# Performance work log

Measured on AMD Instinct MI355X. Metric: run time of the kernel, lower is better.

## Reference

```python
import jax, jax.numpy as jnp
import numpy as np

WIN = (2, 7, 7)  # (H, W, D) window size

def _relative_position_index(H, W, D):
    coords = np.stack(np.meshgrid(np.arange(H), np.arange(W), np.arange(D), indexing='ij'))
    cf = coords.reshape(3, -1)  # [3, N]
    rel = cf[:, :, None] - cf[:, None, :]  # [3, N, N]
    rel = rel.transpose(1, 2, 0).copy()
    rel[:, :, 0] += H - 1
    rel[:, :, 1] += W - 1
    rel[:, :, 2] += D - 1
    rel[:, :, 0] *= (2 * W - 1) * (2 * D - 1)
    rel[:, :, 1] *= 2 * D - 1
    return jnp.asarray(rel.sum(-1), dtype=jnp.int32)  # [N, N]

def setup_inputs() -> dict:
    key = jax.random.key(0)
    ks = jax.random.split(key, 7)
    H, W, D = WIN
    N = H * W * D          # 98
    C = 192
    nh = 6
    num_windows = 64
    B_ = 8 * num_windows   # 512
    x = jax.random.normal(ks[0], (B_, N, C), dtype=jnp.float32)
    # shifted-window attention mask: 0 for allowed pairs, -100 for masked
    mask = jnp.where(jax.random.uniform(ks[1], (num_windows, N, N)) < 0.9, 0.0, -100.0).astype(jnp.float32)
    qkv_w = jax.random.normal(ks[2], (3 * C, C), dtype=jnp.float32) * 0.02
    qkv_b = jnp.zeros((3 * C,), dtype=jnp.float32)
    out_w = jax.random.normal(ks[3], (C, C), dtype=jnp.float32) * 0.02
    out_b = jnp.zeros((C,), dtype=jnp.float32)
    table_len = (2 * H - 1) * (2 * W - 1) * (2 * D - 1)  # 507
    bias_table = jax.random.normal(ks[4], (table_len, nh), dtype=jnp.float32) * 0.02
    rel_index = _relative_position_index(H, W, D)
    return {"x": x, "mask": mask, "qkv_w": qkv_w, "qkv_b": qkv_b,
            "out_w": out_w, "out_b": out_b, "bias_table": bias_table,
            "rel_index": rel_index}

def reference(x, mask, qkv_w, qkv_b, out_w, out_b, bias_table, rel_index):
    B_, N, C = x.shape
    nh = bias_table.shape[1]
    d = C // nh
    scale = d ** (-0.5)
    qkv = (x @ qkv_w.T + qkv_b).reshape(B_, N, 3, nh, d)
    qkv = qkv.transpose(2, 0, 3, 1, 4)          # [3, B_, nh, N, d]
    q, k, v = qkv[0], qkv[1], qkv[2]
    attn = jnp.einsum('bhnd,bhmd->bhnm', q, k) * scale   # [B_, nh, N, N]
    bias = bias_table[rel_index]                 # [N, N, nh]
    attn = attn + bias.transpose(2, 0, 1)[None]  # add relative position bias
    nw = mask.shape[0]
    attn = attn.reshape(B_ // nw, nw, nh, N, N) + mask[None, :, None]
    attn = attn.reshape(B_, nh, N, N)
    p = jax.nn.softmax(attn, axis=-1)
    out = jnp.einsum('bhnm,bhmd->bhnd', p, v)    # [B_, nh, N, d]
    out = out.transpose(0, 2, 1, 3).reshape(B_, N, C)
    return out @ out_w.T + out_b
```

## Files before the change

### kernel.cpp

```cpp
#include <hip/hip_runtime.h>

typedef __attribute__((ext_vector_type(8))) __bf16 bf16x8;
typedef __attribute__((ext_vector_type(4))) float f32x4;
typedef __attribute__((ext_vector_type(8))) unsigned short us8;
typedef __attribute__((ext_vector_type(4))) unsigned short us4;

#define NTOK 98
#define NPAD 112
#define CDIM 192
#define NH 6
#define HD 32
#define NWIN 64
#define BWIN 512
#define MROWS (BWIN * NTOK)
#define QKVN (3 * CDIM)
#define SCALE 0.17677669529663687f

__device__ __forceinline__ unsigned short f2b(float f) {
  unsigned u = __builtin_bit_cast(unsigned, f);
  u += 0x7FFFu + ((u >> 16) & 1u);
  return (unsigned short)(u >> 16);
}

__device__ __forceinline__ bf16x8 ldfrag(const unsigned short* p) {
  return __builtin_bit_cast(bf16x8, *(const us8*)p);
}

__global__ __launch_bounds__(256) void k_biasmask(
    const float* __restrict__ mask, const float* __restrict__ table,
    const int* __restrict__ relidx, float* __restrict__ bm) {
  int idx = blockIdx.x * 256 + threadIdx.x;
  if (idx >= NWIN * NH * NTOK * NTOK) return;
  int j = idx % NTOK;
  int t = idx / NTOK;
  int i = t % NTOK;
  t /= NTOK;
  int h = t % NH;
  int w = t / NH;
  bm[idx] = table[relidx[i * NTOK + j] * NH + h] + mask[(w * NTOK + i) * NTOK + j];
}

__global__ __launch_bounds__(256) void k_qkv(
    const float* __restrict__ x, const float* __restrict__ w,
    const float* __restrict__ bias, unsigned short* __restrict__ qkv) {
  __shared__ unsigned short As[128 * 200];
  __shared__ unsigned short Bs[64 * 200];
  const int tid = threadIdx.x;
  const int m0 = blockIdx.x * 128;
  for (int it = 0; it < 24; ++it) {
    int q = it * 256 + tid;
    int row = q / 48, c4 = q - row * 48;
    float4 v = *(const float4*)(x + (m0 + row) * CDIM + c4 * 4);
    us4 u = {f2b(v.x), f2b(v.y), f2b(v.z), f2b(v.w)};
    *(us4*)&As[row * 200 + c4 * 4] = u;
  }
  const int lane = tid & 63;
  const int l15 = lane & 15, hi = lane >> 4;
  const int wr = (tid >> 6) >> 1, wc = (tid >> 6) & 1;
  __syncthreads();
  for (int j = 0; j < 9; ++j) {
    for (int it = 0; it < 12; ++it) {
      int q = it * 256 + tid;
      int row = q / 48, c4 = q - row * 48;
      float4 v = *(const float4*)(w + (j * 64 + row) * CDIM + c4 * 4);
      us4 u = {f2b(v.x), f2b(v.y), f2b(v.z), f2b(v.w)};
      *(us4*)&Bs[row * 200 + c4 * 4] = u;
    }
    __syncthreads();
    f32x4 acc[4][2];
#pragma unroll
    for (int fr = 0; fr < 4; ++fr) { acc[fr][0] = (f32x4)0.f; acc[fr][1] = (f32x4)0.f; }
#pragma unroll
    for (int ks = 0; ks < 6; ++ks) {
      int k0 = ks * 32 + hi * 8;
      bf16x8 b0 = ldfrag(&Bs[(wc * 32 + l15) * 200 + k0]);
      bf16x8 b1 = ldfrag(&Bs[(wc * 32 + 16 + l15) * 200 + k0]);
#pragma unroll
      for (int fr = 0; fr < 4; ++fr) {
        bf16x8 a = ldfrag(&As[(wr * 64 + fr * 16 + l15) * 200 + k0]);
        acc[fr][0] = __builtin_amdgcn_mfma_f32_16x16x32_bf16(a, b0, acc[fr][0], 0, 0, 0);
        acc[fr][1] = __builtin_amdgcn_mfma_f32_16x16x32_bf16(a, b1, acc[fr][1], 0, 0, 0);
      }
    }
    __syncthreads();
#pragma unroll
    for (int fr = 0; fr < 4; ++fr)
#pragma unroll
      for (int fc = 0; fc < 2; ++fc)
#pragma unroll
        for (int r = 0; r < 4; ++r) {
          int row = m0 + wr * 64 + fr * 16 + hi * 4 + r;
          int col = j * 64 + wc * 32 + fc * 16 + l15;
          float v = acc[fr][fc][r] + bias[col];
          if (col < CDIM) v *= SCALE;
          qkv[row * QKVN + col] = f2b(v);
        }
  }
}

__global__ __launch_bounds__(448) void k_attn(
    const unsigned short* __restrict__ qkv, const float* __restrict__ bm,
    unsigned short* __restrict__ ao) {
  __shared__ unsigned short Ks[NPAD * 40];
  __shared__ unsigned short Vt[32 * 136];
  __shared__ unsigned short P[NPAD * 136];
  const int tid = threadIdx.x;
  const int h = blockIdx.x % NH;
  const int b = blockIdx.x / NH;
  const int wnd = b & (NWIN - 1);
  const int lane = tid & 63, wv = tid >> 6;
  const int l15 = lane & 15, hi = lane >> 4;
  {
    int row = tid >> 2, q = tid & 3;
    us8 kv = (us8)0;
    if (row < NTOK)
      kv = *(const us8*)(qkv + (b * NTOK + row) * QKVN + CDIM + h * HD + q * 8);
    *(us8*)&Ks[row * 40 + q * 8] = kv;
    if (row < NTOK) {
      us8 vv = *(const us8*)(qkv + (b * NTOK + row) * QKVN + 2 * CDIM + h * HD + q * 8);
#pragma unroll
      for (int i = 0; i < 8; ++i) Vt[(q * 8 + i) * 136 + row] = vv[i];
    }
    for (int i = tid; i < 32 * 38; i += 448) {
      int dd = i / 38, n = NTOK + (i - dd * 38);
      Vt[dd * 136 + n] = 0;
    }
    for (int i = tid; i < NPAD * 16; i += 448)
      P[(i >> 4) * 136 + 112 + (i & 15)] = 0;
  }
  int qn = wv * 16 + l15;
  us8 qu = (us8)0;
  if (qn < NTOK)
    qu = *(const us8*)(qkv + (b * NTOK + qn) * QKVN + h * HD + hi * 8);
  bf16x8 qf = __builtin_bit_cast(bf16x8, qu);
  __syncthreads();
  f32x4 sacc[7];
#pragma unroll
  for (int tc = 0; tc < 7; ++tc) {
    bf16x8 kb = ldfrag(&Ks[(tc * 16 + l15) * 40 + hi * 8]);
    sacc[tc] = __builtin_amdgcn_mfma_f32_16x16x32_bf16(qf, kb, (f32x4)0.f, 0, 0, 0);
  }
  const float* bmp = bm + (wnd * NH + h) * NTOK * NTOK;
  float rsum[4];
#pragma unroll
  for (int r = 0; r < 4; ++r) {
    int row = wv * 16 + hi * 4 + r;
    float sv[7];
    float m = -1e30f;
#pragma unroll
    for (int tc = 0; tc < 7; ++tc) {
      int col = tc * 16 + l15;
      float val = -1e30f;
      if (col < NTOK && row < NTOK) val = sacc[tc][r] + bmp[row * NTOK + col];
      sv[tc] = val;
      m = fmaxf(m, val);
    }
#pragma unroll
    for (int off = 1; off < 16; off <<= 1) m = fmaxf(m, __shfl_xor(m, off));
    float s = 0.f;
#pragma unroll
    for (int tc = 0; tc < 7; ++tc) {
      float e = __expf(sv[tc] - m);
      s += e;
      P[row * 136 + tc * 16 + l15] = f2b(e);
    }
#pragma unroll
    for (int off = 1; off < 16; off <<= 1) s += __shfl_xor(s, off);
    rsum[r] = s;
  }
  f32x4 oacc[2];
  oacc[0] = (f32x4)0.f; oacc[1] = (f32x4)0.f;
#pragma unroll
  for (int ks = 0; ks < 4; ++ks) {
    int k0 = ks * 32 + hi * 8;
    bf16x8 pa = ldfrag(&P[(wv * 16 + l15) * 136 + k0]);
#pragma unroll
    for (int tc = 0; tc < 2; ++tc) {
      bf16x8 vb = ldfrag(&Vt[(tc * 16 + l15) * 136 + k0]);
      oacc[tc] = __builtin_amdgcn_mfma_f32_16x16x32_bf16(pa, vb, oacc[tc], 0, 0, 0);
    }
  }
#pragma unroll
  for (int tc = 0; tc < 2; ++tc)
#pragma unroll
    for (int r = 0; r < 4; ++r) {
      int row = wv * 16 + hi * 4 + r;
      if (row < NTOK) {
        float v = oacc[tc][r] / rsum[r];
        ao[(b * NTOK + row) * CDIM + h * HD + tc * 16 + l15] = f2b(v);
      }
    }
}

__global__ __launch_bounds__(256) void k_proj(
    const unsigned short* __restrict__ a, const float* __restrict__ w,
    const float* __restrict__ bias, float* __restrict__ out) {
  __shared__ unsigned short As[128 * 200];
  __shared__ unsigned short Bs[64 * 200];
  const int tid = threadIdx.x;
  const int m0 = blockIdx.x * 128;
  for (int it = 0; it < 12; ++it) {
    int q = it * 256 + tid;
    int row = q / 24, c8 = q - row * 24;
    *(us8*)&As[row * 200 + c8 * 8] = *(const us8*)(a + (m0 + row) * CDIM + c8 * 8);
  }
  const int lane = tid & 63;
  const int l15 = lane & 15, hi = lane >> 4;
  const int wr = (tid >> 6) >> 1, wc = (tid >> 6) & 1;
  __syncthreads();
  for (int j = 0; j < 3; ++j) {
    for (int it = 0; it < 12; ++it) {
      int q = it * 256 + tid;
      int row = q / 48, c4 = q - row * 48;
      float4 v = *(const float4*)(w + (j * 64 + row) * CDIM + c4 * 4);
      us4 u = {f2b(v.x), f2b(v.y), f2b(v.z), f2b(v.w)};
      *(us4*)&Bs[row * 200 + c4 * 4] = u;
    }
    __syncthreads();
    f32x4 acc[4][2];
#pragma unroll
    for (int fr = 0; fr < 4; ++fr) { acc[fr][0] = (f32x4)0.f; acc[fr][1] = (f32x4)0.f; }
#pragma unroll
    for (int ks = 0; ks < 6; ++ks) {
      int k0 = ks * 32 + hi * 8;
      bf16x8 b0 = ldfrag(&Bs[(wc * 32 + l15) * 200 + k0]);
      bf16x8 b1 = ldfrag(&Bs[(wc * 32 + 16 + l15) * 200 + k0]);
#pragma unroll
      for (int fr = 0; fr < 4; ++fr) {
        bf16x8 aa = ldfrag(&As[(wr * 64 + fr * 16 + l15) * 200 + k0]);
        acc[fr][0] = __builtin_amdgcn_mfma_f32_16x16x32_bf16(aa, b0, acc[fr][0], 0, 0, 0);
        acc[fr][1] = __builtin_amdgcn_mfma_f32_16x16x32_bf16(aa, b1, acc[fr][1], 0, 0, 0);
      }
    }
    __syncthreads();
#pragma unroll
    for (int fr = 0; fr < 4; ++fr)
#pragma unroll
      for (int fc = 0; fc < 2; ++fc)
#pragma unroll
        for (int r = 0; r < 4; ++r) {
          int row = m0 + wr * 64 + fr * 16 + hi * 4 + r;
          int col = j * 64 + wc * 32 + fc * 16 + l15;
          out[row * CDIM + col] = acc[fr][fc][r] + bias[col];
        }
  }
}

extern "C" void kernel_launch(void* const* d_in, const int* in_sizes, int n_in,
                              void* d_out, int out_size, void* d_ws, size_t ws_size,
                              hipStream_t stream) {
  const float* x      = (const float*)d_in[0];
  const float* mask   = (const float*)d_in[1];
  const float* qkv_w  = (const float*)d_in[2];
  const float* qkv_b  = (const float*)d_in[3];
  const float* out_w  = (const float*)d_in[4];
  const float* out_b  = (const float*)d_in[5];
  const float* table  = (const float*)d_in[6];
  const int*   relidx = (const int*)d_in[7];
  float* out = (float*)d_out;
  char* ws = (char*)d_ws;

  const size_t bm_bytes  = (size_t)NWIN * NH * NTOK * NTOK * 4;
  const size_t qkv_bytes = (size_t)MROWS * QKVN * 2;
  float* bm = (float*)ws;
  unsigned short* qkvp = (unsigned short*)(ws + bm_bytes);
  unsigned short* aop  = (unsigned short*)(ws + bm_bytes + qkv_bytes);

  int bmtot = NWIN * NH * NTOK * NTOK;
  k_biasmask<<<(bmtot + 255) / 256, 256, 0, stream>>>(mask, table, relidx, bm);
  k_qkv<<<MROWS / 128, 256, 0, stream>>>(x, qkv_w, qkv_b, qkvp);
  k_attn<<<BWIN * NH, 448, 0, stream>>>(qkvp, bm, aop);
  k_proj<<<MROWS / 128, 256, 0, stream>>>(aop, out_w, out_b, out);
}
```

Baseline: 220.6 us.

## Drop materialized bias+mask tensor, pre-convert weights to bf16, head-major QKV layout

Replaces the per-window fused bias+mask tensor (64x6x98x98 floats) with a small per-head bias table plus direct reads of the original mask inside the attention kernel, removing a large write-then-read pass. Weights are converted to bf16 once in a prep kernel so the GEMM blocks load half the bytes and skip repeated conversion. QKV output is stored head-major so attention reads contiguous 64-byte rows per head. In exchange, the attention kernel does two global loads per score instead of one, and the QKV epilogue stores are strided by head.

```diff
diff --git a/kernel.cpp b/kernel.cpp
--- a/kernel.cpp
+++ b/kernel.cpp
@@ -14,7 +14,13 @@
 #define BWIN 512
 #define MROWS (BWIN * NTOK)
 #define QKVN (3 * CDIM)
+#define NN (NTOK * NTOK)
 #define SCALE 0.17677669529663687f
+
+#define PREP_BIAS (NH * NN)
+#define PREP_WQ (QKVN * CDIM)
+#define PREP_WO (CDIM * CDIM)
+#define PREP_TOT (PREP_BIAS + PREP_WQ + PREP_WO)
 
 __device__ __forceinline__ unsigned short f2b(float f) {
   unsigned u = __builtin_bit_cast(unsigned, f);
@@ -26,22 +32,25 @@
   return __builtin_bit_cast(bf16x8, *(const us8*)p);
 }
 
-__global__ __launch_bounds__(256) void k_biasmask(
-    const float* __restrict__ mask, const float* __restrict__ table,
-    const int* __restrict__ relidx, float* __restrict__ bm) {
+__global__ __launch_bounds__(256) void k_prep(
+    const float* __restrict__ table, const int* __restrict__ relidx,
+    const float* __restrict__ wq, const float* __restrict__ wo,
+    float* __restrict__ biasHT, unsigned short* __restrict__ wqb,
+    unsigned short* __restrict__ wob) {
   int idx = blockIdx.x * 256 + threadIdx.x;
-  if (idx >= NWIN * NH * NTOK * NTOK) return;
-  int j = idx % NTOK;
-  int t = idx / NTOK;
-  int i = t % NTOK;
-  t /= NTOK;
-  int h = t % NH;
-  int w = t / NH;
-  bm[idx] = table[relidx[i * NTOK + j] * NH + h] + mask[(w * NTOK + i) * NTOK + j];
+  if (idx < PREP_BIAS) {
+    int h = idx / NN, ij = idx - h * NN;
+    biasHT[idx] = table[relidx[ij] * NH + h];
+    return;
+  }
+  int i2 = idx - PREP_BIAS;
+  if (i2 < PREP_WQ) { if (i2 >= 0) wqb[i2] = f2b(wq[i2]); return; }
+  int i3 = i2 - PREP_WQ;
+  if (i3 < PREP_WO) wob[i3] = f2b(wo[i3]);
 }
 
 __global__ __launch_bounds__(256) void k_qkv(
-    const float* __restrict__ x, const float* __restrict__ w,
+    const float* __restrict__ x, const unsigned short* __restrict__ wqb,
     const float* __restrict__ bias, unsigned short* __restrict__ qkv) {
   __shared__ unsigned short As[128 * 200];
   __shared__ unsigned short Bs[64 * 200];
@@ -59,12 +68,10 @@
   const int wr = (tid >> 6) >> 1, wc = (tid >> 6) & 1;
   __syncthreads();
   for (int j = 0; j < 9; ++j) {
-    for (int it = 0; it < 12; ++it) {
+    for (int it = 0; it < 6; ++it) {
       int q = it * 256 + tid;
-      int row = q / 48, c4 = q - row * 48;
-      float4 v = *(const float4*)(w + (j * 64 + row) * CDIM + c4 * 4);
-      us4 u = {f2b(v.x), f2b(v.y), f2b(v.z), f2b(v.w)};
-      *(us4*)&Bs[row * 200 + c4 * 4] = u;
+      int row = q / 24, c8 = q - row * 24;
+      *(us8*)&Bs[row * 200 + c8 * 8] = *(const us8*)(wqb + (j * 64 + row) * CDIM + c8 * 8);
     }
     __syncthreads();
     f32x4 acc[4][2];
@@ -86,21 +93,26 @@
 #pragma unroll
     for (int fr = 0; fr < 4; ++fr)
 #pragma unroll
-      for (int fc = 0; fc < 2; ++fc)
+      for (int fc = 0; fc < 2; ++fc) {
+        int colb = j * 64 + wc * 32 + fc * 16;
+        int t = (colb >= 2 * CDIM) ? 2 : (colb >= CDIM ? 1 : 0);
+        int head = (colb >> 5) - t * NH;
+        int d = (colb & 31) + l15;
+        long pbase = ((long)(t * NH + head) * MROWS) * 32 + d;
 #pragma unroll
         for (int r = 0; r < 4; ++r) {
           int row = m0 + wr * 64 + fr * 16 + hi * 4 + r;
-          int col = j * 64 + wc * 32 + fc * 16 + l15;
-          float v = acc[fr][fc][r] + bias[col];
-          if (col < CDIM) v *= SCALE;
-          qkv[row * QKVN + col] = f2b(v);
+          float v = acc[fr][fc][r] + bias[colb + l15];
+          if (t == 0) v *= SCALE;
+          qkv[pbase + (long)row * 32] = f2b(v);
         }
+      }
   }
 }
 
 __global__ __launch_bounds__(448) void k_attn(
-    const unsigned short* __restrict__ qkv, const float* __restrict__ bm,
-    unsigned short* __restrict__ ao) {
+    const unsigned short* __restrict__ qkv, const float* __restrict__ biasHT,
+    const float* __restrict__ mask, unsigned short* __restrict__ ao) {
   __shared__ unsigned short Ks[NPAD * 40];
   __shared__ unsigned short Vt[32 * 136];
   __shared__ unsigned short P[NPAD * 136];
@@ -110,14 +122,17 @@
   const int wnd = b & (NWIN - 1);
   const int lane = tid & 63, wv = tid >> 6;
   const int l15 = lane & 15, hi = lane >> 4;
+  const long rb = (long)b * NTOK;
+  const unsigned short* qp = qkv + ((long)h * MROWS + rb) * 32;
+  const unsigned short* kp = qkv + ((long)(NH + h) * MROWS + rb) * 32;
+  const unsigned short* vp = qkv + ((long)(2 * NH + h) * MROWS + rb) * 32;
   {
     int row = tid >> 2, q = tid & 3;
     us8 kv = (us8)0;
-    if (row < NTOK)
-      kv = *(const us8*)(qkv + (b * NTOK + row) * QKVN + CDIM + h * HD + q * 8);
+    if (row < NTOK) kv = *(const us8*)(kp + row * 32 + q * 8);
     *(us8*)&Ks[row * 40 + q * 8] = kv;
     if (row < NTOK) {
-      us8 vv = *(const us8*)(qkv + (b * NTOK + row) * QKVN + 2 * CDIM + h * HD + q * 8);
+      us8 vv = *(const us8*)(vp + row * 32 + q * 8);
 #pragma unroll
       for (int i = 0; i < 8; ++i) Vt[(q * 8 + i) * 136 + row] = vv[i];
     }
@@ -130,8 +145,7 @@
   }
   int qn = wv * 16 + l15;
   us8 qu = (us8)0;
-  if (qn < NTOK)
-    qu = *(const us8*)(qkv + (b * NTOK + qn) * QKVN + h * HD + hi * 8);
+  if (qn < NTOK) qu = *(const us8*)(qp + qn * 32 + hi * 8);
   bf16x8 qf = __builtin_bit_cast(bf16x8, qu);
   __syncthreads();
   f32x4 sacc[7];
@@ -140,7 +154,8 @@
     bf16x8 kb = ldfrag(&Ks[(tc * 16 + l15) * 40 + hi * 8]);
     sacc[tc] = __builtin_amdgcn_mfma_f32_16x16x32_bf16(qf, kb, (f32x4)0.f, 0, 0, 0);
   }
-  const float* bmp = bm + (wnd * NH + h) * NTOK * NTOK;
+  const float* bp = biasHT + h * NN;
+  const float* mp = mask + wnd * NN;
   float rsum[4];
 #pragma unroll
   for (int r = 0; r < 4; ++r) {
@@ -151,7 +166,10 @@
     for (int tc = 0; tc < 7; ++tc) {
       int col = tc * 16 + l15;
       float val = -1e30f;
-      if (col < NTOK && row < NTOK) val = sacc[tc][r] + bmp[row * NTOK + col];
+      if (col < NTOK && row < NTOK) {
+        int o = row * NTOK + col;
+        val = (sacc[tc][r] + bp[o]) + mp[o];
+      }
       sv[tc] = val;
       m = fmaxf(m, val);
     }
@@ -187,13 +205,13 @@
       int row = wv * 16 + hi * 4 + r;
       if (row < NTOK) {
         float v = oacc[tc][r] / rsum[r];
-        ao[(b * NTOK + row) * CDIM + h * HD + tc * 16 + l15] = f2b(v);
+        ao[(rb + row) * CDIM + h * HD + tc * 16 + l15] = f2b(v);
       }
     }
 }
 
 __global__ __launch_bounds__(256) void k_proj(
-    const unsigned short* __restrict__ a, const float* __restrict__ w,
+    const unsigned short* __restrict__ a, const unsigned short* __restrict__ wob,
     const float* __restrict__ bias, float* __restrict__ out) {
   __shared__ unsigned short As[128 * 200];
   __shared__ unsigned short Bs[64 * 200];
@@ -209,12 +227,10 @@
   const int wr = (tid >> 6) >> 1, wc = (tid >> 6) & 1;
   __syncthreads();
   for (int j = 0; j < 3; ++j) {
-    for (int it = 0; it < 12; ++it) {
+    for (int it = 0; it < 6; ++it) {
       int q = it * 256 + tid;
-      int row = q / 48, c4 = q - row * 48;
-      float4 v = *(const float4*)(w + (j * 64 + row) * CDIM + c4 * 4);
-      us4 u = {f2b(v.x), f2b(v.y), f2b(v.z), f2b(v.w)};
-      *(us4*)&Bs[row * 200 + c4 * 4] = u;
+      int row = q / 24, c8 = q - row * 24;
+      *(us8*)&Bs[row * 200 + c8 * 8] = *(const us8*)(wob + (j * 64 + row) * CDIM + c8 * 8);
     }
     __syncthreads();
     f32x4 acc[4][2];
@@ -260,15 +276,20 @@
   float* out = (float*)d_out;
   char* ws = (char*)d_ws;
 
-  const size_t bm_bytes  = (size_t)NWIN * NH * NTOK * NTOK * 4;
-  const size_t qkv_bytes = (size_t)MROWS * QKVN * 2;
-  float* bm = (float*)ws;
-  unsigned short* qkvp = (unsigned short*)(ws + bm_bytes);
-  unsigned short* aop  = (unsigned short*)(ws + bm_bytes + qkv_bytes);
-
-  int bmtot = NWIN * NH * NTOK * NTOK;
-  k_biasmask<<<(bmtot + 255) / 256, 256, 0, stream>>>(mask, table, relidx, bm);
-  k_qkv<<<MROWS / 128, 256, 0, stream>>>(x, qkv_w, qkv_b, qkvp);
-  k_attn<<<BWIN * NH, 448, 0, stream>>>(qkvp, bm, aop);
-  k_proj<<<MROWS / 128, 256, 0, stream>>>(aop, out_w, out_b, out);
-}
+  const size_t off_bias = 0;
+  const size_t off_wqb  = 230656;
+  const size_t off_wob  = 451840;
+  const size_t off_qkv  = 525568;
+  const size_t off_ao   = off_qkv + 57802752;
+  float* biasHT = (float*)(ws + off_bias);
+  unsigned short* wqb  = (unsigned short*)(ws + off_wqb);
+  unsigned short* wob  = (unsigned short*)(ws + off_wob);
+  unsigned short* qkvp = (unsigned short*)(ws + off_qkv);
+  unsigned short* aop  = (unsigned short*)(ws + off_ao);
+
+  k_prep<<<(PREP_TOT + 255) / 256, 256, 0, stream>>>(table, relidx, qkv_w, out_w,
+                                                     biasHT, wqb, wob);
+  k_qkv<<<MROWS / 128, 256, 0, stream>>>(x, wqb, qkv_b, qkvp);
+  k_attn<<<BWIN * NH, 448, 0, stream>>>(qkvp, biasHT, mask, aop);
+  k_proj<<<MROWS / 128, 256, 0, stream>>>(aop, wob, out_b, out);
+}
```

New measurement: 198.2 us. 1.11x faster.
